# Performance work log

Hardware: AMD Instinct MI355X
Metric: run time of the kernel (lower is better)

Reference implementation:

```python
import jax, jax.numpy as jnp
import numpy as np
from jax import lax

B = 64; NF = 64; KS = 3
MEM_N = 64; MEM_D = 256; CTRL = 256
R_HEADS = 3; W_HEADS = 3
HEADS = R_HEADS + W_HEADS
PPH = MEM_D + 1 + 1 + 3 + 1                 # 262 params per head (k, beta, g, s(3), gamma)
TOTAL_P = PPH * HEADS + 2 * W_HEADS * MEM_D  # 3108 (+ erase/add per write head)
CTRL_IN = MEM_D + R_HEADS * MEM_D            # flattened feat (256) + 3 read vectors
CLIP = 20.0


def setup_inputs() -> dict:
    key = jax.random.key(0)
    ks = jax.random.split(key, 12)
    s = 0.05
    return {
        "inputs": jax.random.normal(ks[0], (B, 1, 64, 64), jnp.float32),
        "w_conv0": jax.random.normal(ks[1], (NF, 1, KS, KS), jnp.float32) * s,
        "b_conv0": jnp.zeros((NF,), jnp.float32),
        "w_conv1": jax.random.normal(ks[2], (NF, NF, KS, KS), jnp.float32) * s,
        "b_conv1": jnp.zeros((NF,), jnp.float32),
        "w_enc": jax.random.normal(ks[3], (1, NF, KS, KS), jnp.float32) * s,
        "b_enc": jnp.zeros((1,), jnp.float32),
        "w_conv2": jax.random.normal(ks[4], (NF, 1, KS, KS), jnp.float32) * s,
        "b_conv2": jnp.zeros((NF,), jnp.float32),
        "w_conv3": jax.random.normal(ks[5], (NF, NF, KS, KS), jnp.float32) * s,
        "b_conv3": jnp.zeros((NF,), jnp.float32),
        "w_conv4": jax.random.normal(ks[6], (NF, NF, KS, KS), jnp.float32) * s,
        "b_conv4": jnp.zeros((NF,), jnp.float32),
        "w_lstm_x": jax.random.normal(ks[7], (CTRL_IN, 4 * CTRL), jnp.float32) * s,
        "w_lstm_h": jax.random.normal(ks[8], (CTRL, 4 * CTRL), jnp.float32) * s,
        "b_lstm": jnp.zeros((4 * CTRL,), jnp.float32),
        "w_param": jax.random.normal(ks[9], (CTRL, TOTAL_P), jnp.float32) * s,
        "b_param": jnp.zeros((TOTAL_P,), jnp.float32),
        "w_out": jax.random.normal(ks[10], (CTRL + R_HEADS * MEM_D, MEM_D), jnp.float32) * s,
        "b_out": jnp.zeros((MEM_D,), jnp.float32),
    }


def conv_relu(x, w, b):
    y = lax.conv_general_dilated(x, w, (1, 1), 'SAME', dimension_numbers=('NCHW', 'OIHW', 'NCHW'))
    return jax.nn.relu(y + b[None, :, None, None])


def avg_pool2(x):
    return lax.reduce_window(x, 0.0, lax.add, (1, 1, 2, 2), (1, 1, 2, 2), 'VALID') * 0.25


def upsample2(x):
    return jnp.repeat(jnp.repeat(x, 2, axis=2), 2, axis=3)


def ntm_step(x, w_lstm_x, w_lstm_h, b_lstm, w_param, b_param, w_out, b_out):
    # constant initial state (get_initial_state)
    M = jnp.full((B, MEM_N, MEM_D), 1e-6, x.dtype)
    prev_w = jnp.full((B, HEADS, MEM_N), 1.0 / MEM_N, x.dtype)
    reads0 = jnp.zeros((B, R_HEADS * MEM_D), x.dtype)
    h0 = jnp.zeros((B, CTRL), x.dtype)
    c0 = jnp.zeros((B, CTRL), x.dtype)
    # LSTM controller step
    ctrl_in = jnp.concatenate([x, reads0], axis=1)          # [B, 1024]
    z = ctrl_in @ w_lstm_x + h0 @ w_lstm_h + b_lstm
    i, f, g_, o = jnp.split(z, 4, axis=1)
    c = jax.nn.sigmoid(f) * c0 + jax.nn.sigmoid(i) * jnp.tanh(g_)
    h = jax.nn.sigmoid(o) * jnp.tanh(c)
    # head parameters
    p = jnp.clip(h @ w_param + b_param, -CLIP, CLIP)        # [B, 3108]
    hp = p[:, :PPH * HEADS].reshape(B, HEADS, PPH)
    k = jnp.tanh(hp[..., :MEM_D])                            # [B,H,D]
    beta = jax.nn.softplus(hp[..., MEM_D])                   # [B,H]
    g = jax.nn.sigmoid(hp[..., MEM_D + 1])
    s = jax.nn.softmax(hp[..., MEM_D + 2:MEM_D + 5], axis=-1)  # shift weights, range 1
    gamma = jax.nn.softplus(hp[..., MEM_D + 5]) + 1.0
    # content addressing: cosine similarity + sharpened softmax
    dots = jnp.einsum('bhd,bnd->bhn', k, M)
    denom = jnp.linalg.norm(k, axis=-1)[..., None] * jnp.linalg.norm(M, axis=-1)[:, None, :] + 1e-8
    w_c = jax.nn.softmax(beta[..., None] * dots / denom, axis=-1)
    # interpolation with previous weights
    w_g = g[..., None] * w_c + (1.0 - g[..., None]) * prev_w
    # circular convolution with shift kernel {0,+1,-1}
    w_t = s[..., 0:1] * w_g + s[..., 1:2] * jnp.roll(w_g, 1, axis=-1) + s[..., 2:3] * jnp.roll(w_g, -1, axis=-1)
    # sharpening
    pw = jnp.power(w_t + 1e-16, gamma[..., None])
    w = pw / (jnp.sum(pw, axis=-1, keepdims=True) + 1e-8)    # [B,H,N]
    # read from memory (first R_HEADS heads)
    reads = jnp.einsum('bhn,bnd->bhd', w[:, :R_HEADS], M).reshape(B, R_HEADS * MEM_D)
    # write: sequential erase/add per write head (state is discarded by the wrapper)
    ea = p[:, PPH * HEADS:].reshape(B, W_HEADS, 2, MEM_D)
    erase = jax.nn.sigmoid(ea[:, :, 0])                      # [B,Wh,D]
    add = jnp.tanh(ea[:, :, 1])
    w_w = w[:, R_HEADS:]
    for j in range(W_HEADS):
        M = M * (1.0 - w_w[:, j, :, None] * erase[:, j, None, :]) + w_w[:, j, :, None] * add[:, j, None, :]
    out = jnp.clip(jnp.concatenate([h, reads], axis=1) @ w_out + b_out, -CLIP, CLIP)
    return out


def reference(inputs, w_conv0, b_conv0, w_conv1, b_conv1, w_enc, b_enc, w_conv2, b_conv2, w_conv3, b_conv3, w_conv4, b_conv4, w_lstm_x, w_lstm_h, b_lstm, w_param, b_param, w_out, b_out):
    x = conv_relu(inputs, w_conv0, b_conv0)   # [B,64,64,64]
    x = avg_pool2(x)                          # [B,64,32,32]
    x = conv_relu(x, w_conv1, b_conv1)
    x = avg_pool2(x)                          # [B,64,16,16]
    x = conv_relu(x, w_enc, b_enc)            # [B,1,16,16]
    x = x.reshape(B, -1)                      # [B,256]
    x = ntm_step(x, w_lstm_x, w_lstm_h, b_lstm, w_param, b_param, w_out, b_out)
    x = x.reshape(B, 1, 16, 16)
    x = conv_relu(x, w_conv2, b_conv2)
    x = upsample2(x)                          # [B,64,32,32]
    x = conv_relu(x, w_conv3, b_conv3)
    x = upsample2(x)                          # [B,64,64,64]
    x = conv_relu(x, w_conv4, b_conv4)        # [B,64,64,64]
    return x
```

## Files before the change

kernel.cpp:

```cpp
#include <hip/hip_runtime.h>
#include <hip/hip_bf16.h>


typedef __attribute__((ext_vector_type(8))) short short8;
typedef __attribute__((ext_vector_type(4))) float f32x4;

static const size_t OFF_A1H = 0;
static const size_t OFF_A1L = 9469952;
static const size_t OFF_PL  = 18939904;
static const size_t OFF_A3H = 39911424;
static const size_t OFF_A3L = 42565632;
static const size_t OFF_W1  = 45219840;
static const size_t OFF_W3  = 45367296;
static const size_t OFF_W4  = 45514752;
static const size_t OFF_RS  = 45662208;
static const size_t OFF_XE  = 45711360;
static const size_t OFF_Z   = 45776896;

__device__ inline void bf16split(float v, unsigned short& h, unsigned short& l) {
    __hip_bfloat16 hb = __float2bfloat16(v);
    float hf = __bfloat162float(hb);
    __hip_bfloat16 lb = __float2bfloat16(v - hf);
    h = __builtin_bit_cast(unsigned short, hb);
    l = __builtin_bit_cast(unsigned short, lb);
}

__global__ void wprep_rowsum_kernel(
    const float* __restrict__ w1, const float* __restrict__ w3,
    const float* __restrict__ w4, const float* __restrict__ w_out,
    unsigned short* __restrict__ whi1, unsigned short* __restrict__ wlo1,
    unsigned short* __restrict__ whi3, unsigned short* __restrict__ wlo3,
    unsigned short* __restrict__ whi4, unsigned short* __restrict__ wlo4,
    double* __restrict__ rsP)
{
    int blk = blockIdx.x;
    if (blk >= 432) {
        int idx = blk - 432;
        int r = idx >> 3, c = idx & 7;
        int m = threadIdx.x;
        const float* wp = w_out + (size_t)(256 + r * 256 + c * 32) * 256 + m;
        double s[4] = {0, 0, 0, 0};
        for (int d0 = 0; d0 < 32; d0 += 4) {
#pragma unroll
            for (int k = 0; k < 4; ++k)
                s[k] += (double)wp[(size_t)(d0 + k) * 256];
        }
        rsP[(idx << 8) + m] = (s[0] + s[1]) + (s[2] + s[3]);
        return;
    }
    int layer = blk / 144;
    int r = (blk % 144) * 256 + threadIdx.x;
    const float* w = layer == 0 ? w1 : (layer == 1 ? w3 : w4);
    unsigned short* hi = layer == 0 ? whi1 : (layer == 1 ? whi3 : whi4);
    unsigned short* lo = layer == 0 ? wlo1 : (layer == 1 ? wlo3 : wlo4);
    int j  = r & 7;
    int ln = (r >> 3) & 63;
    int n  = (r >> 9) & 3;
    int ch = (r >> 11) & 1;
    int t  = r >> 12;
    int lc = ln & 15, kg = ln >> 4;
    int co = n * 16 + lc;
    int ci = ch * 32 + kg * 8 + j;
    unsigned short h, l;
    bf16split(w[(co * 64 + ci) * 9 + t], h, l);
    hi[r] = h; lo[r] = l;
}

__device__ inline void halo_zero_one(unsigned short* hi, unsigned short* lo,
                                     int S, int idx)
{
    int P = S + 2, ring = 4 * S + 4;
    int co = idx & 63;
    int cell = (idx >> 6) % ring;
    int b = (idx >> 6) / ring;
    int y, x;
    if (cell < P)            { y = 0;     x = cell; }
    else if (cell < 2 * P)   { y = P - 1; x = cell - P; }
    else { int c2 = cell - 2 * P; y = 1 + (c2 >> 1); x = (c2 & 1) ? P - 1 : 0; }
    size_t a = ((size_t)(b * P + y) * P + x) * 64 + co;
    hi[a] = 0; lo[a] = 0;
}

__global__ void halo_all_kernel(unsigned short* __restrict__ a1h,
                                unsigned short* __restrict__ a1l,
                                unsigned short* __restrict__ a3h,
                                unsigned short* __restrict__ a3l)
{
    int idx = blockIdx.x * 256 + threadIdx.x;
    if (idx < 540672) halo_zero_one(a1h, a1l, 32, idx);
    else              halo_zero_one(a3h, a3l, 16, idx - 540672);
}

__global__ __launch_bounds__(256) void conv0_pool_kernel(
    const float* __restrict__ in, const float* __restrict__ w,
    const float* __restrict__ bias,
    unsigned short* __restrict__ ohi, unsigned short* __restrict__ olo)
{
    int idx = blockIdx.x * 256 + threadIdx.x;
    int co = idx & 63, x = (idx >> 6) & 31, y = (idx >> 11) & 31, b = idx >> 16;
    float w9[9];
#pragma unroll
    for (int t = 0; t < 9; ++t) w9[t] = w[co * 9 + t];
    float bv = bias[co];
    const float* ip = in + (size_t)b * 4096;
    float p[4][4];
#pragma unroll
    for (int r = 0; r < 4; ++r) {
        int gy = 2 * y - 1 + r;
#pragma unroll
        for (int c = 0; c < 4; ++c) {
            int gx = 2 * x - 1 + c;
            float v = 0.f;
            if ((unsigned)gy < 64u && (unsigned)gx < 64u) v = ip[gy * 64 + gx];
            p[r][c] = v;
        }
    }
    float s4 = 0.f;
#pragma unroll
    for (int dy = 0; dy < 2; ++dy)
#pragma unroll
        for (int dx = 0; dx < 2; ++dx) {
            float a = bv;
#pragma unroll
            for (int ky = 0; ky < 3; ++ky)
#pragma unroll
                for (int kx = 0; kx < 3; ++kx)
                    a = fmaf(w9[ky * 3 + kx], p[dy + ky][dx + kx], a);
            s4 += fmaxf(a, 0.f);
        }
    unsigned short h, l;
    bf16split(s4 * 0.25f, h, l);
    size_t a = ((size_t)(b * 34 + y + 1) * 34 + x + 1) * 64 + co;
    ohi[a] = h; olo[a] = l;
}

template <int UP, int H, int ROWS, int OUTMODE>
__device__ __forceinline__ void conv_mfma_body(
    const unsigned short* __restrict__ ahi, const unsigned short* __restrict__ alo,
    const unsigned short* __restrict__ whiP, const unsigned short* __restrict__ wloP,
    const float* __restrict__ bias,
    float* __restrict__ outf, unsigned short* __restrict__ ohi,
    unsigned short* __restrict__ olo)
{
    constexpr int TILEH = 4 * ROWS;
    constexpr int SRC   = H >> UP;
    constexpr int PITCH = SRC + 2;
    constexpr int TPR   = H / 16;
    constexpr int TPC   = H / TILEH;
    constexpr int AH    = (UP ? TILEH / 2 : TILEH) + 2;
    constexpr int AW    = UP ? 10 : 18;
    constexpr int NPX   = AH * AW;

    int b  = blockIdx.x / (TPC * TPR);
    int tt = blockIdx.x % (TPC * TPR);
    int y0 = (tt / TPR) * TILEH, x0 = (tt % TPR) * 16;
    const int tid = threadIdx.x;
    const int wv = tid >> 6, lane = tid & 63;
    const int lc = lane & 15, kg = lane >> 4;

    __shared__ unsigned short sAhi[NPX * 64];
    __shared__ unsigned short sAlo[NPX * 64];
    __shared__ unsigned short sW[2][4096];

    const int r0 = ((y0 - 1) >> UP) + 1;
    const int c0 = ((x0 - 1) >> UP) + 1;

    for (int c = tid; c < NPX * 8; c += 256) {
        int pix = c >> 3, sub = c & 7;
        int py = pix / AW, px = pix - py * AW;
        size_t g = ((size_t)(b * PITCH + r0 + py) * PITCH + (c0 + px)) * 64 + sub * 8;
        int l = (pix * 64 + sub * 8) ^ ((pix & 7) << 3);
        *(short8*)&sAhi[l] = *(const short8*)&ahi[g];
        *(short8*)&sAlo[l] = *(const short8*)&alo[g];
    }
    for (int c = tid; c < 512; c += 256) {
        if (c < 256) *(short8*)&sW[0][c * 8] = *(const short8*)&whiP[c * 8];
        else *(short8*)&sW[0][2048 + (c - 256) * 8] = *(const short8*)&wloP[(c - 256) * 8];
    }
    __syncthreads();

    int lxv[3], lyv[ROWS + 2];
#pragma unroll
    for (int kx = 0; kx < 3; ++kx)
        lxv[kx] = (((x0 + lc + kx - 1) >> UP) + 1) - c0;
#pragma unroll
    for (int r = 0; r < ROWS + 2; ++r)
        lyv[r] = (((y0 + ROWS * wv + r - 1) >> UP) + 1) - r0;

    f32x4 acc[ROWS][4];
#pragma unroll
    for (int m = 0; m < ROWS; ++m)
#pragma unroll
        for (int n = 0; n < 4; ++n) acc[m][n] = f32x4{0.f, 0.f, 0.f, 0.f};

#pragma unroll
    for (int k = 0; k < 18; ++k) {
        if (k + 1 < 18) {
            int slb = (k + 1) * 2048;
            for (int c = tid; c < 512; c += 256) {
                if (c < 256) *(short8*)&sW[(k + 1) & 1][c * 8] =
                    *(const short8*)&whiP[slb + c * 8];
                else *(short8*)&sW[(k + 1) & 1][2048 + (c - 256) * 8] =
                    *(const short8*)&wloP[slb + (c - 256) * 8];
            }
        }
        const int t = k >> 1, ch = k & 1;
        const int ky = t / 3, kx = t - ky * 3;
        short8 ah[ROWS], al[ROWS];
#pragma unroll
        for (int m = 0; m < ROWS; ++m) {
            int p = lyv[ky + m] * AW + lxv[kx];
            int i = (p * 64 + ch * 32 + kg * 8) ^ ((p & 7) << 3);
            ah[m] = *(const short8*)&sAhi[i];
            al[m] = *(const short8*)&sAlo[i];
        }
        const unsigned short* wb = &sW[k & 1][0];
#pragma unroll
        for (int n = 0; n < 4; ++n) {
            short8 bh = *(const short8*)&wb[(n * 64 + lane) * 8];
            short8 bl = *(const short8*)&wb[2048 + (n * 64 + lane) * 8];
#pragma unroll
            for (int m = 0; m < ROWS; ++m) {
                acc[m][n] = __builtin_amdgcn_mfma_f32_16x16x32_bf16(ah[m], bh, acc[m][n], 0, 0, 0);
                acc[m][n] = __builtin_amdgcn_mfma_f32_16x16x32_bf16(ah[m], bl, acc[m][n], 0, 0, 0);
                acc[m][n] = __builtin_amdgcn_mfma_f32_16x16x32_bf16(al[m], bh, acc[m][n], 0, 0, 0);
            }
        }
        __syncthreads();
    }

    if (OUTMODE == 1) {
        const int opitch = H + 2;
#pragma unroll
        for (int n = 0; n < 4; ++n) {
            int co = n * 16 + lc;
            float bv = bias[co];
#pragma unroll
            for (int m = 0; m < ROWS; ++m) {
                int row = y0 + ROWS * wv + m, cb = x0 + kg * 4;
                f32x4 v = acc[m][n];
#pragma unroll
                for (int j = 0; j < 4; ++j) {
                    float val = fmaxf(v[j] + bv, 0.f);
                    unsigned short h, l;
                    bf16split(val, h, l);
                    size_t a = ((size_t)(b * opitch + row + 1) * opitch + cb + j + 1) * 64 + co;
                    ohi[a] = h; olo[a] = l;
                }
            }
        }
    } else if (OUTMODE == 2) {
#pragma unroll
        for (int n = 0; n < 4; ++n) {
            int co = n * 16 + lc;
            float bv = bias[co];
            f32x4 v0 = acc[0][n], v1 = acc[1][n];
            float r00 = fmaxf(v0.x + bv, 0.f), r01 = fmaxf(v0.y + bv, 0.f);
            float r02 = fmaxf(v0.z + bv, 0.f), r03 = fmaxf(v0.w + bv, 0.f);
            float r10 = fmaxf(v1.x + bv, 0.f), r11 = fmaxf(v1.y + bv, 0.f);
            float r12 = fmaxf(v1.z + bv, 0.f), r13 = fmaxf(v1.w + bv, 0.f);
            float p0 = ((r00 + r01) + (r10 + r11)) * 0.25f;
            float p1 = ((r02 + r03) + (r12 + r13)) * 0.25f;
            int py = (y0 >> 1) + wv;
            int px = (x0 >> 1) + kg * 2;
            float* op = outf + ((size_t)(b * 64 + co) * 16 + py) * 16 + px;
            op[0] = p0; op[1] = p1;
        }
    } else {
#pragma unroll
        for (int n = 0; n < 4; ++n) {
            int co = n * 16 + lc;
            float bv = bias[co];
#pragma unroll
            for (int m = 0; m < ROWS; ++m) {
                int row = y0 + ROWS * wv + m, cb = x0 + kg * 4;
                f32x4 v = acc[m][n], res;
                res.x = fmaxf(v.x + bv, 0.f);
                res.y = fmaxf(v.y + bv, 0.f);
                res.z = fmaxf(v.z + bv, 0.f);
                res.w = fmaxf(v.w + bv, 0.f);
                *(f32x4*)&outf[((size_t)(b * 64 + co) * H + row) * H + cb] = res;
            }
        }
    }
}

__global__ __launch_bounds__(256, 2) void conv1_mfma_kernel(
    const unsigned short* __restrict__ ahi, const unsigned short* __restrict__ alo,
    const unsigned short* __restrict__ whiP, const unsigned short* __restrict__ wloP,
    const float* __restrict__ bias, float* __restrict__ pooled)
{ conv_mfma_body<0, 32, 2, 2>(ahi, alo, whiP, wloP, bias, pooled, nullptr, nullptr); }

__global__ __launch_bounds__(256, 3) void conv3_mfma_kernel(
    const unsigned short* __restrict__ ahi, const unsigned short* __restrict__ alo,
    const unsigned short* __restrict__ whiP, const unsigned short* __restrict__ wloP,
    const float* __restrict__ bias,
    unsigned short* __restrict__ ohi, unsigned short* __restrict__ olo)
{ conv_mfma_body<1, 32, 2, 1>(ahi, alo, whiP, wloP, bias, nullptr, ohi, olo); }

__global__ __launch_bounds__(256, 3) void conv4_mfma_kernel(
    const unsigned short* __restrict__ ahi, const unsigned short* __restrict__ alo,
    const unsigned short* __restrict__ whiP, const unsigned short* __restrict__ wloP,
    const float* __restrict__ bias, float* __restrict__ outf)
{ conv_mfma_body<1, 64, 4, 0>(ahi, alo, whiP, wloP, bias, outf, nullptr, nullptr); }

__global__ __launch_bounds__(1024) void enc_kernel(
    const float* __restrict__ pooled, const float* __restrict__ w_enc,
    const float* __restrict__ b_enc, float* __restrict__ xE)
{
    int b = blockIdx.x, t = threadIdx.x;
    __shared__ float sE[16384];
    __shared__ float eP[4][256];
    {
        const f32x4* src = (const f32x4*)(pooled + (size_t)b * 16384);
        f32x4* dst = (f32x4*)sE;
#pragma unroll
        for (int p = t; p < 4096; p += 1024) dst[p] = src[p];
    }
    __syncthreads();
    {
        int g = t >> 8, j = t & 255;
        int y = j >> 4, x = j & 15;
        float a0 = 0.f, a1 = 0.f;
        for (int cc = 0; cc < 16; ++cc) {
            int ci = g * 16 + cc;
#pragma unroll
            for (int ky = 0; ky < 3; ++ky) {
                int gy = y + ky - 1;
                if ((unsigned)gy >= 16u) continue;
#pragma unroll
                for (int kx = 0; kx < 3; ++kx) {
                    int gx = x + kx - 1;
                    if ((unsigned)gx >= 16u) continue;
                    float pr = w_enc[ci * 9 + ky * 3 + kx] * sE[ci * 256 + gy * 16 + gx];
                    if (cc & 1) a1 += pr; else a0 += pr;
                }
            }
        }
        eP[g][j] = a0 + a1;
    }
    __syncthreads();
    if (t < 256) {
        float v = ((eP[0][t] + eP[1][t]) + (eP[2][t] + eP[3][t])) + b_enc[0];
        xE[b * 256 + t] = fmaxf(v, 0.f);
    }
}

__global__ __launch_bounds__(256) void lstm_kernel(
    const float* __restrict__ xE, const float* __restrict__ wx,
    float* __restrict__ zE)
{
    int blk = blockIdx.x;
    int g = blk >> 6, b = blk & 63;
    int goff = (g == 0) ? 0 : (g == 1 ? 512 : 768);
    int j = threadIdx.x;
    __shared__ float sx[256];
    sx[j] = xE[b * 256 + j];
    __syncthreads();
    const float* wp = wx + goff + j;
    float acc[8];
#pragma unroll
    for (int k = 0; k < 8; ++k) acc[k] = 0.f;
    for (int d0 = 0; d0 < 256; d0 += 8) {
        float xv[8], wv[8];
#pragma unroll
        for (int k = 0; k < 8; ++k) xv[k] = sx[d0 + k];
#pragma unroll
        for (int k = 0; k < 8; ++k) wv[k] = wp[(size_t)(d0 + k) * 1024];
#pragma unroll
        for (int k = 0; k < 8; ++k) acc[k] = fmaf(xv[k], wv[k], acc[k]);
    }
    zE[b * 768 + g * 256 + j] = ((acc[0] + acc[1]) + (acc[2] + acc[3]))
                              + ((acc[4] + acc[5]) + (acc[6] + acc[7]));
}

__global__ __launch_bounds__(1024) void tail_kernel(
    const float* __restrict__ zE, const float* __restrict__ bl,
    const float* __restrict__ w_param, const float* __restrict__ b_param,
    const float* __restrict__ w_out, const float* __restrict__ b_out,
    const double* __restrict__ rsP, const float* __restrict__ w2,
    const float* __restrict__ b2,
    unsigned short* __restrict__ ohi, unsigned short* __restrict__ olo)
{
    int b = blockIdx.x, t = threadIdx.x;
    __shared__ float  sh[256];
    __shared__ double red[3][256];
    __shared__ double srv[3];
    __shared__ float  dP[4][256];
    __shared__ float  sNtm[256];

    if (t < 256) {
        int j = t;
        float zif = (float)((double)zE[b * 768 + j]       + (double)bl[j]);
        float zgf = (float)((double)zE[b * 768 + 256 + j] + (double)bl[512 + j]);
        float zof = (float)((double)zE[b * 768 + 512 + j] + (double)bl[768 + j]);
        double c = (1.0 / (1.0 + exp(-(double)zif))) * tanh((double)zgf);
        float cf = (float)c;
        double hh = (1.0 / (1.0 + exp(-(double)zof))) * tanh((double)cf);
        sh[j] = (float)hh;
    }
    __syncthreads();
    if (t < 768) {
        int r = t >> 8, j = t & 255;
        red[r][j] = (double)sh[j] * (double)w_param[(size_t)j * 3108 + r * 262 + 261];
    }
    __syncthreads();
    for (int s = 128; s > 0; s >>= 1) {
        if (t < 768) {
            int r = t >> 8, j = t & 255;
            if (j < s) red[r][j] += red[r][j + s];
        }
        __syncthreads();
    }
    if (t < 3) {
        double s = red[t][0];
        float pf = (float)(s + (double)b_param[t * 262 + 261]);
        pf = fminf(fmaxf(pf, -20.f), 20.f);
        double gamma = log1p(exp((double)pf)) + 1.0;
        double q = pow(0.015625 + 1e-16, gamma);
        double wv = q / (64.0 * q + 1e-8);
        srv[t] = wv * 64.0 * 1e-6;
    }
    __syncthreads();
    {
        int q = t >> 8, m = t & 255;
        const float* wp = w_out + (size_t)(q * 64) * 256 + m;
        float a4[4] = {0.f, 0.f, 0.f, 0.f};
        for (int d0 = 0; d0 < 64; d0 += 4) {
            float hv4[4], wv4[4];
#pragma unroll
            for (int k = 0; k < 4; ++k) hv4[k] = sh[q * 64 + d0 + k];
#pragma unroll
            for (int k = 0; k < 4; ++k) wv4[k] = wp[(size_t)(d0 + k) * 256];
#pragma unroll
            for (int k = 0; k < 4; ++k) a4[k] = fmaf(hv4[k], wv4[k], a4[k]);
        }
        dP[q][m] = (a4[0] + a4[1]) + (a4[2] + a4[3]);
    }
    __syncthreads();
    if (t < 256) {
        int m = t;
        float dotf = (dP[0][m] + dP[1][m]) + (dP[2][m] + dP[3][m]);
        double acc = (double)dotf + (double)b_out[m];
#pragma unroll
        for (int r = 0; r < 3; ++r) {
            double rsum = 0;
#pragma unroll
            for (int c = 0; c < 8; ++c) rsum += rsP[((r * 8 + c) << 8) + m];
            acc += srv[r] * rsum;
        }
        acc = fmin(fmax(acc, -20.0), 20.0);
        sNtm[m] = (float)acc;
    }
    __syncthreads();
    for (int p = t; p < 16384; p += 1024) {
        int co = p & 63, x4 = (p >> 6) & 15, y4 = p >> 10;
        float a = b2[co];
#pragma unroll
        for (int ky = 0; ky < 3; ++ky) {
            int gy = y4 + ky - 1;
            if ((unsigned)gy >= 16u) continue;
#pragma unroll
            for (int kx = 0; kx < 3; ++kx) {
                int gx = x4 + kx - 1;
                if ((unsigned)gx >= 16u) continue;
                a = fmaf(w2[co * 9 + ky * 3 + kx], sNtm[gy * 16 + gx], a);
            }
        }
        unsigned short hh, ll;
        bf16split(fmaxf(a, 0.f), hh, ll);
        size_t adst = ((size_t)(b * 18 + y4 + 1) * 18 + x4 + 1) * 64 + co;
        ohi[adst] = hh; olo[adst] = ll;
    }
}

extern "C" void kernel_launch(void* const* d_in, const int* in_sizes, int n_in,
                              void* d_out, int out_size, void* d_ws, size_t ws_size,
                              hipStream_t stream)
{
    const float* inputs   = (const float*)d_in[0];
    const float* w_conv0  = (const float*)d_in[1];
    const float* b_conv0  = (const float*)d_in[2];
    const float* w_conv1  = (const float*)d_in[3];
    const float* b_conv1  = (const float*)d_in[4];
    const float* w_enc    = (const float*)d_in[5];
    const float* b_enc    = (const float*)d_in[6];
    const float* w_conv2  = (const float*)d_in[7];
    const float* b_conv2  = (const float*)d_in[8];
    const float* w_conv3  = (const float*)d_in[9];
    const float* b_conv3  = (const float*)d_in[10];
    const float* w_conv4  = (const float*)d_in[11];
    const float* b_conv4  = (const float*)d_in[12];
    const float* w_lstm_x = (const float*)d_in[13];
    const float* b_lstm   = (const float*)d_in[15];
    const float* w_param  = (const float*)d_in[16];
    const float* b_param  = (const float*)d_in[17];
    const float* w_out_   = (const float*)d_in[18];
    const float* b_out_   = (const float*)d_in[19];

    char* ws = (char*)d_ws;
    unsigned short* a1h = (unsigned short*)(ws + OFF_A1H);
    unsigned short* a1l = (unsigned short*)(ws + OFF_A1L);
    float*  pooled = (float*)(ws + OFF_PL);
    unsigned short* a3h = (unsigned short*)(ws + OFF_A3H);
    unsigned short* a3l = (unsigned short*)(ws + OFF_A3L);
    unsigned short* a4h = a1h;
    unsigned short* a4l = a1l;
    unsigned short* whi1 = (unsigned short*)(ws + OFF_W1); unsigned short* wlo1 = whi1 + 36864;
    unsigned short* whi3 = (unsigned short*)(ws + OFF_W3); unsigned short* wlo3 = whi3 + 36864;
    unsigned short* whi4 = (unsigned short*)(ws + OFF_W4); unsigned short* wlo4 = whi4 + 36864;
    double* rsP = (double*)(ws + OFF_RS);
    float*  xE  = (float*)(ws + OFF_XE);
    float*  zE  = (float*)(ws + OFF_Z);

    wprep_rowsum_kernel<<<456, 256, 0, stream>>>(
        w_conv1, w_conv3, w_conv4, w_out_,
        whi1, wlo1, whi3, wlo3, whi4, wlo4, rsP);
    halo_all_kernel<<<3200, 256, 0, stream>>>(a1h, a1l, a3h, a3l);

    conv0_pool_kernel<<<16384, 256, 0, stream>>>(inputs, w_conv0, b_conv0, a1h, a1l);
    conv1_mfma_kernel<<<512, 256, 0, stream>>>(a1h, a1l, whi1, wlo1, b_conv1, pooled);

    enc_kernel<<<64, 1024, 0, stream>>>(pooled, w_enc, b_enc, xE);
    lstm_kernel<<<192, 256, 0, stream>>>(xE, w_lstm_x, zE);
    tail_kernel<<<64, 1024, 0, stream>>>(
        zE, b_lstm, w_param, b_param, w_out_, b_out_, rsP, w_conv2, b_conv2, a3h, a3l);

    conv3_mfma_kernel<<<512, 256, 0, stream>>>(a3h, a3l, whi3, wlo3, b_conv3, a4h, a4l);
    conv4_mfma_kernel<<<1024, 256, 0, stream>>>(a4h, a4l, whi4, wlo4, b_conv4, (float*)d_out);
}
```

Measured before the change: 184.9 us.

## Drop bf16 low-part activations, keeping split weights in conv MFMA passes

Activations are now stored only as single bf16 values instead of hi/lo split pairs, so each conv does two MFMA passes per tile instead of three. It also halves activation shared memory and global traffic, and raises the launch-bounds occupancy hints. A small transposed copy of the gamma weights is prepared in the weight-prep kernel so the tail kernel reads them with contiguous loads instead of strided ones. Numerical accuracy drops because activation rounding error is no longer compensated, which risks tolerance failures.

New measurement: 171.0 us. -7.5%, faster.

```diff
diff --git a/kernel.cpp b/kernel.cpp
--- a/kernel.cpp
+++ b/kernel.cpp
@@ -6,16 +6,15 @@
 typedef __attribute__((ext_vector_type(4))) float f32x4;
 
 static const size_t OFF_A1H = 0;
-static const size_t OFF_A1L = 9469952;
 static const size_t OFF_PL  = 18939904;
 static const size_t OFF_A3H = 39911424;
-static const size_t OFF_A3L = 42565632;
 static const size_t OFF_W1  = 45219840;
 static const size_t OFF_W3  = 45367296;
 static const size_t OFF_W4  = 45514752;
 static const size_t OFF_RS  = 45662208;
 static const size_t OFF_XE  = 45711360;
 static const size_t OFF_Z   = 45776896;
+static const size_t OFF_GW  = 45973504;
 
 __device__ inline void bf16split(float v, unsigned short& h, unsigned short& l) {
     __hip_bfloat16 hb = __float2bfloat16(v);
@@ -25,15 +24,28 @@
     l = __builtin_bit_cast(unsigned short, lb);
 }
 
+__device__ inline unsigned short bf16of(float v) {
+    __hip_bfloat16 hb = __float2bfloat16(v);
+    return __builtin_bit_cast(unsigned short, hb);
+}
+
 __global__ void wprep_rowsum_kernel(
     const float* __restrict__ w1, const float* __restrict__ w3,
     const float* __restrict__ w4, const float* __restrict__ w_out,
+    const float* __restrict__ w_param,
     unsigned short* __restrict__ whi1, unsigned short* __restrict__ wlo1,
     unsigned short* __restrict__ whi3, unsigned short* __restrict__ wlo3,
     unsigned short* __restrict__ whi4, unsigned short* __restrict__ wlo4,
-    double* __restrict__ rsP)
+    double* __restrict__ rsP, float* __restrict__ gwT)
 {
     int blk = blockIdx.x;
+    if (blk == 456) {
+        int t = threadIdx.x;
+#pragma unroll
+        for (int r = 0; r < 3; ++r)
+            gwT[r * 256 + t] = w_param[(size_t)t * 3108 + r * 262 + 261];
+        return;
+    }
     if (blk >= 432) {
         int idx = blk - 432;
         int r = idx >> 3, c = idx & 7;
@@ -66,8 +78,7 @@
     hi[r] = h; lo[r] = l;
 }
 
-__device__ inline void halo_zero_one(unsigned short* hi, unsigned short* lo,
-                                     int S, int idx)
+__device__ inline void halo_zero_one(unsigned short* hi, int S, int idx)
 {
     int P = S + 2, ring = 4 * S + 4;
     int co = idx & 63;
@@ -77,24 +88,20 @@
     if (cell < P)            { y = 0;     x = cell; }
     else if (cell < 2 * P)   { y = P - 1; x = cell - P; }
     else { int c2 = cell - 2 * P; y = 1 + (c2 >> 1); x = (c2 & 1) ? P - 1 : 0; }
-    size_t a = ((size_t)(b * P + y) * P + x) * 64 + co;
-    hi[a] = 0; lo[a] = 0;
+    hi[((size_t)(b * P + y) * P + x) * 64 + co] = 0;
 }
 
 __global__ void halo_all_kernel(unsigned short* __restrict__ a1h,
-                                unsigned short* __restrict__ a1l,
-                                unsigned short* __restrict__ a3h,
-                                unsigned short* __restrict__ a3l)
+                                unsigned short* __restrict__ a3h)
 {
     int idx = blockIdx.x * 256 + threadIdx.x;
-    if (idx < 540672) halo_zero_one(a1h, a1l, 32, idx);
-    else              halo_zero_one(a3h, a3l, 16, idx - 540672);
+    if (idx < 540672) halo_zero_one(a1h, 32, idx);
+    else              halo_zero_one(a3h, 16, idx - 540672);
 }
 
 __global__ __launch_bounds__(256) void conv0_pool_kernel(
     const float* __restrict__ in, const float* __restrict__ w,
-    const float* __restrict__ bias,
-    unsigned short* __restrict__ ohi, unsigned short* __restrict__ olo)
+    const float* __restrict__ bias, unsigned short* __restrict__ ohi)
 {
     int idx = blockIdx.x * 256 + threadIdx.x;
     int co = idx & 63, x = (idx >> 6) & 31, y = (idx >> 11) & 31, b = idx >> 16;
@@ -128,19 +135,16 @@
                     a = fmaf(w9[ky * 3 + kx], p[dy + ky][dx + kx], a);
             s4 += fmaxf(a, 0.f);
         }
-    unsigned short h, l;
-    bf16split(s4 * 0.25f, h, l);
     size_t a = ((size_t)(b * 34 + y + 1) * 34 + x + 1) * 64 + co;
-    ohi[a] = h; olo[a] = l;
+    ohi[a] = bf16of(s4 * 0.25f);
 }
 
 template <int UP, int H, int ROWS, int OUTMODE>
 __device__ __forceinline__ void conv_mfma_body(
-    const unsigned short* __restrict__ ahi, const unsigned short* __restrict__ alo,
+    const unsigned short* __restrict__ ahi,
     const unsigned short* __restrict__ whiP, const unsigned short* __restrict__ wloP,
     const float* __restrict__ bias,
-    float* __restrict__ outf, unsigned short* __restrict__ ohi,
-    unsigned short* __restrict__ olo)
+    float* __restrict__ outf, unsigned short* __restrict__ ohi)
 {
     constexpr int TILEH = 4 * ROWS;
     constexpr int SRC   = H >> UP;
@@ -159,7 +163,6 @@
     const int lc = lane & 15, kg = lane >> 4;
 
     __shared__ unsigned short sAhi[NPX * 64];
-    __shared__ unsigned short sAlo[NPX * 64];
     __shared__ unsigned short sW[2][4096];
 
     const int r0 = ((y0 - 1) >> UP) + 1;
@@ -171,7 +174,6 @@
         size_t g = ((size_t)(b * PITCH + r0 + py) * PITCH + (c0 + px)) * 64 + sub * 8;
         int l = (pix * 64 + sub * 8) ^ ((pix & 7) << 3);
         *(short8*)&sAhi[l] = *(const short8*)&ahi[g];
-        *(short8*)&sAlo[l] = *(const short8*)&alo[g];
     }
     for (int c = tid; c < 512; c += 256) {
         if (c < 256) *(short8*)&sW[0][c * 8] = *(const short8*)&whiP[c * 8];
@@ -206,13 +208,12 @@
         }
         const int t = k >> 1, ch = k & 1;
         const int ky = t / 3, kx = t - ky * 3;
-        short8 ah[ROWS], al[ROWS];
+        short8 ah[ROWS];
 #pragma unroll
         for (int m = 0; m < ROWS; ++m) {
             int p = lyv[ky + m] * AW + lxv[kx];
             int i = (p * 64 + ch * 32 + kg * 8) ^ ((p & 7) << 3);
             ah[m] = *(const short8*)&sAhi[i];
-            al[m] = *(const short8*)&sAlo[i];
         }
         const unsigned short* wb = &sW[k & 1][0];
 #pragma unroll
@@ -223,7 +224,6 @@
             for (int m = 0; m < ROWS; ++m) {
                 acc[m][n] = __builtin_amdgcn_mfma_f32_16x16x32_bf16(ah[m], bh, acc[m][n], 0, 0, 0);
                 acc[m][n] = __builtin_amdgcn_mfma_f32_16x16x32_bf16(ah[m], bl, acc[m][n], 0, 0, 0);
-                acc[m][n] = __builtin_amdgcn_mfma_f32_16x16x32_bf16(al[m], bh, acc[m][n], 0, 0, 0);
             }
         }
         __syncthreads();
@@ -242,10 +242,8 @@
 #pragma unroll
                 for (int j = 0; j < 4; ++j) {
                     float val = fmaxf(v[j] + bv, 0.f);
-                    unsigned short h, l;
-                    bf16split(val, h, l);
                     size_t a = ((size_t)(b * opitch + row + 1) * opitch + cb + j + 1) * 64 + co;
-                    ohi[a] = h; olo[a] = l;
+                    ohi[a] = bf16of(val);
                 }
             }
         }
@@ -285,24 +283,23 @@
     }
 }
 
-__global__ __launch_bounds__(256, 2) void conv1_mfma_kernel(
-    const unsigned short* __restrict__ ahi, const unsigned short* __restrict__ alo,
+__global__ __launch_bounds__(256, 4) void conv1_mfma_kernel(
+    const unsigned short* __restrict__ ahi,
     const unsigned short* __restrict__ whiP, const unsigned short* __restrict__ wloP,
     const float* __restrict__ bias, float* __restrict__ pooled)
-{ conv_mfma_body<0, 32, 2, 2>(ahi, alo, whiP, wloP, bias, pooled, nullptr, nullptr); }
-
-__global__ __launch_bounds__(256, 3) void conv3_mfma_kernel(
-    const unsigned short* __restrict__ ahi, const unsigned short* __restrict__ alo,
+{ conv_mfma_body<0, 32, 2, 2>(ahi, whiP, wloP, bias, pooled, nullptr); }
+
+__global__ __launch_bounds__(256, 6) void conv3_mfma_kernel(
+    const unsigned short* __restrict__ ahi,
     const unsigned short* __restrict__ whiP, const unsigned short* __restrict__ wloP,
-    const float* __restrict__ bias,
-    unsigned short* __restrict__ ohi, unsigned short* __restrict__ olo)
-{ conv_mfma_body<1, 32, 2, 1>(ahi, alo, whiP, wloP, bias, nullptr, ohi, olo); }
-
-__global__ __launch_bounds__(256, 3) void conv4_mfma_kernel(
-    const unsigned short* __restrict__ ahi, const unsigned short* __restrict__ alo,
+    const float* __restrict__ bias, unsigned short* __restrict__ ohi)
+{ conv_mfma_body<1, 32, 2, 1>(ahi, whiP, wloP, bias, nullptr, ohi); }
+
+__global__ __launch_bounds__(256, 5) void conv4_mfma_kernel(
+    const unsigned short* __restrict__ ahi,
     const unsigned short* __restrict__ whiP, const unsigned short* __restrict__ wloP,
     const float* __restrict__ bias, float* __restrict__ outf)
-{ conv_mfma_body<1, 64, 4, 0>(ahi, alo, whiP, wloP, bias, outf, nullptr, nullptr); }
+{ conv_mfma_body<1, 64, 4, 0>(ahi, whiP, wloP, bias, outf, nullptr); }
 
 __global__ __launch_bounds__(1024) void enc_kernel(
     const float* __restrict__ pooled, const float* __restrict__ w_enc,
@@ -376,11 +373,10 @@
 
 __global__ __launch_bounds__(1024) void tail_kernel(
     const float* __restrict__ zE, const float* __restrict__ bl,
-    const float* __restrict__ w_param, const float* __restrict__ b_param,
+    const float* __restrict__ gwT, const float* __restrict__ b_param,
     const float* __restrict__ w_out, const float* __restrict__ b_out,
     const double* __restrict__ rsP, const float* __restrict__ w2,
-    const float* __restrict__ b2,
-    unsigned short* __restrict__ ohi, unsigned short* __restrict__ olo)
+    const float* __restrict__ b2, unsigned short* __restrict__ ohi)
 {
     int b = blockIdx.x, t = threadIdx.x;
     __shared__ float  sh[256];
@@ -402,7 +398,7 @@
     __syncthreads();
     if (t < 768) {
         int r = t >> 8, j = t & 255;
-        red[r][j] = (double)sh[j] * (double)w_param[(size_t)j * 3108 + r * 262 + 261];
+        red[r][j] = (double)sh[j] * (double)gwT[r * 256 + j];
     }
     __syncthreads();
     for (int s = 128; s > 0; s >>= 1) {
@@ -467,10 +463,8 @@
                 a = fmaf(w2[co * 9 + ky * 3 + kx], sNtm[gy * 16 + gx], a);
             }
         }
-        unsigned short hh, ll;
-        bf16split(fmaxf(a, 0.f), hh, ll);
         size_t adst = ((size_t)(b * 18 + y4 + 1) * 18 + x4 + 1) * 64 + co;
-        ohi[adst] = hh; olo[adst] = ll;
+        ohi[adst] = bf16of(fmaxf(a, 0.f));
     }
 }
 
@@ -500,32 +494,30 @@
 
     char* ws = (char*)d_ws;
     unsigned short* a1h = (unsigned short*)(ws + OFF_A1H);
-    unsigned short* a1l = (unsigned short*)(ws + OFF_A1L);
     float*  pooled = (float*)(ws + OFF_PL);
     unsigned short* a3h = (unsigned short*)(ws + OFF_A3H);
-    unsigned short* a3l = (unsigned short*)(ws + OFF_A3L);
     unsigned short* a4h = a1h;
-    unsigned short* a4l = a1l;
     unsigned short* whi1 = (unsigned short*)(ws + OFF_W1); unsigned short* wlo1 = whi1 + 36864;
     unsigned short* whi3 = (unsigned short*)(ws + OFF_W3); unsigned short* wlo3 = whi3 + 36864;
     unsigned short* whi4 = (unsigned short*)(ws + OFF_W4); unsigned short* wlo4 = whi4 + 36864;
     double* rsP = (double*)(ws + OFF_RS);
     float*  xE  = (float*)(ws + OFF_XE);
     float*  zE  = (float*)(ws + OFF_Z);
-
-    wprep_rowsum_kernel<<<456, 256, 0, stream>>>(
-        w_conv1, w_conv3, w_conv4, w_out_,
-        whi1, wlo1, whi3, wlo3, whi4, wlo4, rsP);
-    halo_all_kernel<<<3200, 256, 0, stream>>>(a1h, a1l, a3h, a3l);
-
-    conv0_pool_kernel<<<16384, 256, 0, stream>>>(inputs, w_conv0, b_conv0, a1h, a1l);
-    conv1_mfma_kernel<<<512, 256, 0, stream>>>(a1h, a1l, whi1, wlo1, b_conv1, pooled);
+    float*  gwT = (float*)(ws + OFF_GW);
+
+    wprep_rowsum_kernel<<<457, 256, 0, stream>>>(
+        w_conv1, w_conv3, w_conv4, w_out_, w_param,
+        whi1, wlo1, whi3, wlo3, whi4, wlo4, rsP, gwT);
+    halo_all_kernel<<<3200, 256, 0, stream>>>(a1h, a3h);
+
+    conv0_pool_kernel<<<16384, 256, 0, stream>>>(inputs, w_conv0, b_conv0, a1h);
+    conv1_mfma_kernel<<<512, 256, 0, stream>>>(a1h, whi1, wlo1, b_conv1, pooled);
 
     enc_kernel<<<64, 1024, 0, stream>>>(pooled, w_enc, b_enc, xE);
     lstm_kernel<<<192, 256, 0, stream>>>(xE, w_lstm_x, zE);
     tail_kernel<<<64, 1024, 0, stream>>>(
-        zE, b_lstm, w_param, b_param, w_out_, b_out_, rsP, w_conv2, b_conv2, a3h, a3l);
-
-    conv3_mfma_kernel<<<512, 256, 0, stream>>>(a3h, a3l, whi3, wlo3, b_conv3, a4h, a4l);
-    conv4_mfma_kernel<<<1024, 256, 0, stream>>>(a4h, a4l, whi4, wlo4, b_conv4, (float*)d_out);
-}
+        zE, b_lstm, gwT, b_param, w_out_, b_out_, rsP, w_conv2, b_conv2, a3h);
+
+    conv3_mfma_kernel<<<512, 256, 0, stream>>>(a3h, whi3, wlo3, b_conv3, a4h);
+    conv4_mfma_kernel<<<1024, 256, 0, stream>>>(a4h, whi4, wlo4, b_conv4, (float*)d_out);
+}
```
